# Optimization experiments

Hardware: AMD Instinct MI355X
Metric: run time of the kernel (lower is better)

The kernel has to match this reference:

```python
import jax, jax.numpy as jnp
import numpy as np

S, B, C = 7, 2, 20
LAMBDA_COORD = 5.0
LAMBDA_NOOBJ = 0.5
WH_EPS = 1e-6
IOU_EPS = 1e-6
BATCH = 16384


def _iou_yolo(a, b):
    # a, b: [..., 4] in (cx, cy, w, h) 'yolo' center format
    ax1, ay1 = a[..., 0] - a[..., 2] / 2, a[..., 1] - a[..., 3] / 2
    ax2, ay2 = a[..., 0] + a[..., 2] / 2, a[..., 1] + a[..., 3] / 2
    bx1, by1 = b[..., 0] - b[..., 2] / 2, b[..., 1] - b[..., 3] / 2
    bx2, by2 = b[..., 0] + b[..., 2] / 2, b[..., 1] + b[..., 3] / 2
    iw = jnp.clip(jnp.minimum(ax2, bx2) - jnp.maximum(ax1, bx1), 0.0)
    ih = jnp.clip(jnp.minimum(ay2, by2) - jnp.maximum(ay1, by1), 0.0)
    inter = iw * ih
    area_a = jnp.abs((ax2 - ax1) * (ay2 - ay1))
    area_b = jnp.abs((bx2 - bx1) * (by2 - by1))
    return inter / (area_a + area_b - inter + IOU_EPS)


def setup_inputs() -> dict:
    key = jax.random.key(0)
    k1, k2, k3 = jax.random.split(key, 3)
    D = C + 5 * B  # 30
    y_trues = jax.random.uniform(k1, (BATCH, S, S, D), dtype=jnp.float32)
    # conf channel must be exactly 0.0 or 1.0 (loss branches on == 1)
    conf = (jax.random.uniform(k2, (BATCH, S, S)) < 0.3).astype(jnp.float32)
    y_trues = y_trues.at[..., 4].set(conf)
    y_preds = jax.random.normal(k3, (BATCH, S, S, D), dtype=jnp.float32)
    return {"y_trues": y_trues, "y_preds": y_preds}


def reference(y_trues, y_preds):
    D = C + 5 * B
    t = y_trues.reshape(-1, S * S, D)   # [N, 49, 30]
    p = y_preds.reshape(-1, S * S, D)
    batch_size = p.shape[0]

    b = t[..., 0:4]
    bhat1 = p[..., 0:4]
    bhat2 = p[..., 5:9]

    iou1 = _iou_yolo(b, bhat1)          # [N, 49]
    iou2 = _iou_yolo(b, bhat2)
    use1 = iou1 > iou2

    bhat = jnp.where(use1[..., None], bhat1, bhat2)            # responsible box
    confhat_chosen = jnp.where(use1, p[..., 4], p[..., 9])
    confhat_other = jnp.where(use1, p[..., 9], p[..., 4])

    # coord losses (object cells)
    xy = LAMBDA_COORD * ((b[..., 0] - bhat[..., 0]) ** 2 + (b[..., 1] - bhat[..., 1]) ** 2)
    wh = LAMBDA_COORD * (
        (jnp.sqrt(b[..., 2]) - jnp.sqrt(jnp.abs(bhat[..., 2] + WH_EPS))) ** 2
        + (jnp.sqrt(b[..., 3]) - jnp.sqrt(jnp.abs(bhat[..., 3] + WH_EPS))) ** 2
    )
    obj_conf = (t[..., 4] - confhat_chosen) ** 2
    noobj_in_obj = LAMBDA_NOOBJ * (0.0 - confhat_other) ** 2
    cls = jnp.sum((t[..., 10:] - p[..., 10:]) ** 2, axis=-1)

    obj_terms = xy + wh + obj_conf + noobj_in_obj + cls

    # no-object cells: penalize both predicted confs toward y_true conf (== target conf channel)
    noobj_terms = LAMBDA_NOOBJ * (
        (t[..., 4] - p[..., 4]) ** 2 + (t[..., 4] - p[..., 9]) ** 2
    )

    obj_mask = t[..., 4] == 1.0
    total = jnp.sum(jnp.where(obj_mask, obj_terms, noobj_terms))
    return total / batch_size
```

## Files before the change

kernel.cpp:

```cpp
#include <hip/hip_runtime.h>

#define LAMBDA_COORD 5.0f
#define LAMBDA_NOOBJ 0.5f
#define WH_EPS 1e-6f
#define IOU_EPS 1e-6f


constexpr int THREADS = 256;

__device__ __forceinline__ float iou_yolo(float a0, float a1, float a2, float a3,
                                          float b0, float b1, float b2, float b3) {
    float ax1 = a0 - a2 * 0.5f, ay1 = a1 - a3 * 0.5f;
    float ax2 = a0 + a2 * 0.5f, ay2 = a1 + a3 * 0.5f;
    float bx1 = b0 - b2 * 0.5f, by1 = b1 - b3 * 0.5f;
    float bx2 = b0 + b2 * 0.5f, by2 = b1 + b3 * 0.5f;
    float iw = fmaxf(fminf(ax2, bx2) - fmaxf(ax1, bx1), 0.0f);
    float ih = fmaxf(fminf(ay2, by2) - fmaxf(ay1, by1), 0.0f);
    float inter = iw * ih;
    float area_a = fabsf((ax2 - ax1) * (ay2 - ay1));
    float area_b = fabsf((bx2 - bx1) * (by2 - by1));
    return inter / (area_a + area_b - inter + IOU_EPS);
}

__device__ __forceinline__ float cell_loss(const float* t, const float* p) {
    const float b0 = t[0], b1 = t[1], b2 = t[2], b3 = t[3], t4 = t[4];

    float iou1 = iou_yolo(b0, b1, b2, b3, p[0], p[1], p[2], p[3]);
    float iou2 = iou_yolo(b0, b1, b2, b3, p[5], p[6], p[7], p[8]);
    bool use1 = iou1 > iou2;

    float bh0 = use1 ? p[0] : p[5];
    float bh1 = use1 ? p[1] : p[6];
    float bh2 = use1 ? p[2] : p[7];
    float bh3 = use1 ? p[3] : p[8];
    float conf_c = use1 ? p[4] : p[9];
    float conf_o = use1 ? p[9] : p[4];

    float dx = b0 - bh0, dy = b1 - bh1;
    float xy = LAMBDA_COORD * (dx * dx + dy * dy);

    float sw = sqrtf(b2) - sqrtf(fabsf(bh2 + WH_EPS));
    float sh = sqrtf(b3) - sqrtf(fabsf(bh3 + WH_EPS));
    float wh = LAMBDA_COORD * (sw * sw + sh * sh);

    float dc = t4 - conf_c;
    float obj_conf = dc * dc;
    float noobj_in_obj = LAMBDA_NOOBJ * conf_o * conf_o;

    float cls = 0.0f;
#pragma unroll
    for (int k = 10; k < 30; ++k) {
        float d = t[k] - p[k];
        cls += d * d;
    }

    float obj_terms = xy + wh + obj_conf + noobj_in_obj + cls;

    float d4 = t4 - p[4], d9 = t4 - p[9];
    float noobj_terms = LAMBDA_NOOBJ * (d4 * d4 + d9 * d9);

    return (t4 == 1.0f) ? obj_terms : noobj_terms;
}

__global__ __launch_bounds__(THREADS, 2) void yolo_loss_main(
    const float4* __restrict__ tv, const float4* __restrict__ pv,
    float* __restrict__ ws, int npairs) {
    const int pair = blockIdx.x * THREADS + threadIdx.x;

    float v = 0.0f;
    if (pair < npairs) {
        const float4* tg = tv + (size_t)pair * 15;
        const float4* pg = pv + (size_t)pair * 15;
        float4 tb[15], pb[15];
#pragma unroll
        for (int j = 0; j < 15; ++j) tb[j] = tg[j];
#pragma unroll
        for (int j = 0; j < 15; ++j) pb[j] = pg[j];
        const float* tf = (const float*)tb;
        const float* pf = (const float*)pb;
        v = cell_loss(tf, pf) + cell_loss(tf + 30, pf + 30);
    }

#pragma unroll
    for (int off = 32; off > 0; off >>= 1)
        v += __shfl_down(v, off, 64);

    __shared__ float part[THREADS / 64];
    if ((threadIdx.x & 63) == 0) part[threadIdx.x >> 6] = v;
    __syncthreads();
    if (threadIdx.x == 0) {
        float s = 0.0f;
#pragma unroll
        for (int w = 0; w < THREADS / 64; ++w) s += part[w];
        ws[blockIdx.x] = s;
    }
}

__global__ __launch_bounds__(256) void yolo_loss_finish(
    const float* __restrict__ ws, float* __restrict__ out,
    int nblocks, float inv_batch) {
    float v = 0.0f;
    for (int i = threadIdx.x; i < nblocks; i += 256) v += ws[i];
#pragma unroll
    for (int off = 32; off > 0; off >>= 1)
        v += __shfl_down(v, off, 64);
    __shared__ float part[4];
    if ((threadIdx.x & 63) == 0) part[threadIdx.x >> 6] = v;
    __syncthreads();
    if (threadIdx.x == 0)
        out[0] = (part[0] + part[1] + part[2] + part[3]) * inv_batch;
}

extern "C" void kernel_launch(void* const* d_in, const int* in_sizes, int n_in,
                              void* d_out, int out_size, void* d_ws, size_t ws_size,
                              hipStream_t stream) {
    const float* t = (const float*)d_in[0];
    const float* p = (const float*)d_in[1];
    float* out = (float*)d_out;
    float* ws = (float*)d_ws;

    const int total = in_sizes[0];
    const int cells = total / 30;
    const int npairs = cells / 2;
    const int batch = cells / 49;
    const float inv_batch = 1.0f / (float)batch;

    const int blocks = (npairs + THREADS - 1) / THREADS;

    yolo_loss_main<<<blocks, THREADS, 0, stream>>>(
        (const float4*)t, (const float4*)p, ws, npairs);
    yolo_loss_finish<<<1, 256, 0, stream>>>(ws, out, blocks, inv_batch);
}
```

Before: 209.5 us.

## Stage tiles into LDS via global_load_lds with coalesced loads, one cell per thread

```diff
diff --git a/kernel.cpp b/kernel.cpp
--- a/kernel.cpp
+++ b/kernel.cpp
@@ -7,6 +7,7 @@
 
 
 constexpr int THREADS = 256;
+constexpr int TILE_VEC4 = 1920;
 
 __device__ __forceinline__ float iou_yolo(float a0, float a1, float a2, float a3,
                                           float b0, float b1, float b2, float b3) {
@@ -62,31 +63,44 @@
     return (t4 == 1.0f) ? obj_terms : noobj_terms;
 }
 
+__device__ __forceinline__ void stage16(const float4* g_lane, float4* l_wave) {
+    __builtin_amdgcn_global_load_lds(
+        (const __attribute__((address_space(1))) void*)g_lane,
+        (__attribute__((address_space(3))) void*)l_wave,
+        16, 0, 0);
+}
+
 __global__ __launch_bounds__(THREADS, 2) void yolo_loss_main(
     const float4* __restrict__ tv, const float4* __restrict__ pv,
-    float* __restrict__ ws, int npairs) {
-    const int pair = blockIdx.x * THREADS + threadIdx.x;
+    float* __restrict__ ws) {
+    __shared__ float4 sbuf[2 * TILE_VEC4];
+    __shared__ float part[THREADS / 64];
 
-    float v = 0.0f;
-    if (pair < npairs) {
-        const float4* tg = tv + (size_t)pair * 15;
-        const float4* pg = pv + (size_t)pair * 15;
-        float4 tb[15], pb[15];
+    const int lane = threadIdx.x & 63;
+    const int wid  = threadIdx.x >> 6;
+    const size_t base = (size_t)blockIdx.x * TILE_VEC4;
+
 #pragma unroll
-        for (int j = 0; j < 15; ++j) tb[j] = tg[j];
-#pragma unroll
-        for (int j = 0; j < 15; ++j) pb[j] = pg[j];
-        const float* tf = (const float*)tb;
-        const float* pf = (const float*)pb;
-        v = cell_loss(tf, pf) + cell_loss(tf + 30, pf + 30);
+    for (int j = 0; j < 15; ++j) {
+        const int idx = j * THREADS + wid * 64;
+        const int myidx = idx + lane;
+        const float4* src = (myidx < TILE_VEC4)
+                          ? (tv + base + myidx)
+                          : (pv + base + (myidx - TILE_VEC4));
+        stage16(src, sbuf + idx);
     }
+
+    __syncthreads();
+
+    const float* st = (const float*)sbuf;
+    const float* sp = (const float*)(sbuf + TILE_VEC4);
+    float v = cell_loss(st + threadIdx.x * 30, sp + threadIdx.x * 30);
 
 #pragma unroll
     for (int off = 32; off > 0; off >>= 1)
         v += __shfl_down(v, off, 64);
 
-    __shared__ float part[THREADS / 64];
-    if ((threadIdx.x & 63) == 0) part[threadIdx.x >> 6] = v;
+    if (lane == 0) part[wid] = v;
     __syncthreads();
     if (threadIdx.x == 0) {
         float s = 0.0f;
@@ -121,13 +135,12 @@
 
     const int total = in_sizes[0];
     const int cells = total / 30;
-    const int npairs = cells / 2;
     const int batch = cells / 49;
     const float inv_batch = 1.0f / (float)batch;
 
-    const int blocks = (npairs + THREADS - 1) / THREADS;
+    const int blocks = cells / THREADS;
 
     yolo_loss_main<<<blocks, THREADS, 0, stream>>>(
-        (const float4*)t, (const float4*)p, ws, npairs);
+        (const float4*)t, (const float4*)p, ws);
     yolo_loss_finish<<<1, 256, 0, stream>>>(ws, out, blocks, inv_batch);
 }
```

Measured after the change: 205.8 us. About the same (-1.7%).
